# Performance work log

Hardware: AMD Instinct MI355X
Metric: run time of the kernel (lower is better)

The kernel has to match this reference:

```python
import jax, jax.numpy as jnp
import numpy as np

D = 1024      # atrybuty (d_model)
H = 16        # kanaly (heads)
DH = D // H   # head dim
B, T = 4, 2048
EPS = 1e-5


def setup_inputs() -> dict:
    key = jax.random.key(0)
    ks = jax.random.split(key, 16)
    s = 0.02
    return {
        "x":  jax.random.normal(ks[0], (B, T, D), jnp.float32),
        "wq": jax.random.normal(ks[1], (D, D), jnp.float32) * s,
        "wk": jax.random.normal(ks[2], (D, D), jnp.float32) * s,
        "wv": jax.random.normal(ks[3], (D, D), jnp.float32) * s,
        "wp": jax.random.normal(ks[4], (D, D), jnp.float32) * s,
        "bp": jnp.zeros((D,), jnp.float32),
        "w1": jax.random.normal(ks[5], (D, 4 * D), jnp.float32) * s,
        "b1": jnp.zeros((4 * D,), jnp.float32),
        "w2": jax.random.normal(ks[6], (4 * D, D), jnp.float32) * s,
        "b2": jnp.zeros((D,), jnp.float32),
        "g1": jnp.ones((D,), jnp.float32),
        "be1": jnp.zeros((D,), jnp.float32),
        "g2": jnp.ones((D,), jnp.float32),
        "be2": jnp.zeros((D,), jnp.float32),
    }


def _layernorm(x, g, b):
    mu = jnp.mean(x, axis=-1, keepdims=True)
    var = jnp.mean(jnp.square(x - mu), axis=-1, keepdims=True)
    return (x - mu) * jax.lax.rsqrt(var + EPS) * g + b


def reference(x, wq, wk, wv, wp, bp, w1, b1, w2, b2, g1, be1, g2, be2):
    b, t, d = x.shape
    # --- self-attention on ln1(x) ---
    h = _layernorm(x, g1, be1)
    # per-head Linears are equivalent to one [D,D] projection split into heads
    q = (h @ wq).reshape(b, t, H, DH).transpose(0, 2, 1, 3)  # [B,H,T,Dh]
    k = (h @ wk).reshape(b, t, H, DH).transpose(0, 2, 1, 3)
    v = (h @ wv).reshape(b, t, H, DH).transpose(0, 2, 1, 3)
    # NOTE: original scales by full embed dim C, not head_dim
    scale = jnp.asarray(d, x.dtype) ** -0.5
    wei = jnp.einsum("bhqd,bhkd->bhqk", q, k) * scale
    causal = jnp.tril(jnp.ones((t, t), bool))
    wei = jnp.where(causal, wei, -jnp.inf)
    wei = jax.nn.softmax(wei, axis=-1)
    att = jnp.einsum("bhqk,bhkd->bhqd", wei, v)
    att = att.transpose(0, 2, 1, 3).reshape(b, t, d)
    x = x + att @ wp + bp
    # --- feedforward on ln2(x) ---
    h2 = _layernorm(x, g2, be2)
    x = x + jax.nn.relu(h2 @ w1 + b1) @ w2 + b2
    return x
```

## Files before the change

kernel.cpp:

```cpp
#include <hip/hip_runtime.h>
#include <hip/hip_bf16.h>
#include <stdint.h>

#define DM   1024
#define NH   16
#define DH   64
#define BATCH 4
#define SEQ  2048
#define MROWS (BATCH*SEQ)

typedef float f32x4 __attribute__((ext_vector_type(4)));
typedef __bf16 bf16x8 __attribute__((ext_vector_type(8)));
typedef short s16x4 __attribute__((ext_vector_type(4)));
typedef int   i32x2 __attribute__((ext_vector_type(2)));

#define QSCALE 0.045084220f

#define VM(n) asm volatile("s_waitcnt vmcnt(" #n ")" ::: "memory")
#define LGKM0 do { asm volatile("s_waitcnt lgkmcnt(0)" ::: "memory"); \
                   __builtin_amdgcn_sched_barrier(0); } while (0)

__device__ __forceinline__ short f2bs(float f) {
    __bf16 h = (__bf16)f;
    return __builtin_bit_cast(short, h);
}

__device__ __forceinline__ void gload_lds16(const void* g, void* l) {
    __builtin_amdgcn_global_load_lds(
        (__attribute__((address_space(1))) void*)(g),
        (__attribute__((address_space(3))) void*)(l), 16, 0, 0);
}

__device__ __forceinline__ void swz_xy(int ny, int& x, int& y) {
    const int bid = blockIdx.x;
    const int cpx = gridDim.x >> 3;
    const int wg  = (bid & 7) * cpx + (bid >> 3);
    x = wg / ny;
    y = wg % ny;
}

__global__ __launch_bounds__(256) void transpose_cvt_kernel(
    const float* __restrict__ w, short* __restrict__ wt, int K, int N)
{
    __shared__ short tile[64 * 65];
    const int k0 = blockIdx.x * 64, n0 = blockIdx.y * 64;
    const int t = threadIdx.x;
#pragma unroll
    for (int i = 0; i < 16; ++i) {
        int idx = i * 256 + t;
        int r = idx >> 6, c = idx & 63;
        tile[r * 65 + c] = f2bs(w[(size_t)(k0 + r) * N + n0 + c]);
    }
    __syncthreads();
#pragma unroll
    for (int i = 0; i < 16; ++i) {
        int idx = i * 256 + t;
        int r = idx >> 6, c = idx & 63;
        wt[(size_t)(n0 + r) * K + k0 + c] = tile[c * 65 + r];
    }
}

__global__ __launch_bounds__(256) void ln_kernel(
    const float* __restrict__ x, const float* __restrict__ g,
    const float* __restrict__ be, short* __restrict__ out)
{
    const int row = blockIdx.x, t = threadIdx.x;
    const float4 v = ((const float4*)(x + (size_t)row * DM))[t];
    float s  = v.x + v.y + v.z + v.w;
    float ss = v.x * v.x + v.y * v.y + v.z * v.z + v.w * v.w;
#pragma unroll
    for (int d = 1; d < 64; d <<= 1) {
        s  += __shfl_xor(s, d, 64);
        ss += __shfl_xor(ss, d, 64);
    }
    __shared__ float red[8];
    const int wid = t >> 6;
    if ((t & 63) == 0) { red[wid] = s; red[wid + 4] = ss; }
    __syncthreads();
    s  = red[0] + red[1] + red[2] + red[3];
    ss = red[4] + red[5] + red[6] + red[7];
    const float mu = s * (1.0f / DM);
    const float rs = rsqrtf(ss * (1.0f / DM) - mu * mu + 1e-5f);
    const float4 gg = ((const float4*)g)[t];
    const float4 bb = ((const float4*)be)[t];
    short4 o;
    o.x = f2bs((v.x - mu) * rs * gg.x + bb.x);
    o.y = f2bs((v.y - mu) * rs * gg.y + bb.y);
    o.z = f2bs((v.z - mu) * rs * gg.z + bb.z);
    o.w = f2bs((v.w - mu) * rs * gg.w + bb.w);
    ((short4*)(out + (size_t)row * DM))[t] = o;
}

template<int NCHUNK>
__device__ __forceinline__ void stage32(
    const short* __restrict__ G, int ldk, int row0, int k0,
    short* __restrict__ lds, int t)
{
#pragma unroll
    for (int i = 0; i < NCHUNK / 512; ++i) {
        const int c  = i * 512 + t;
        const int r  = c >> 2;
        const int sl = (c & 3) ^ ((r >> 1) & 3);
        gload_lds16(&G[(size_t)(row0 + r) * ldk + k0 + sl * 8], &lds[c * 8]);
    }
}

template<int EPI>
__global__ __launch_bounds__(512) void gemm256(
    const short* __restrict__ A, const short* __restrict__ Bt,
    int N, int K, int nyT,
    const float* __restrict__ bias, short* __restrict__ outb,
    short* __restrict__ qo, short* __restrict__ ko, short* __restrict__ vo)
{
    __shared__ short As[4][8192];
    __shared__ short Bs[4][8192];
    const int t = threadIdx.x, lane = t & 63, w = t >> 6;
    const int l15 = lane & 15, hi = lane >> 4;
    const int wm = (w >> 2) * 128, wn = (w & 3) * 64;
    int bx, by; swz_xy(nyT, bx, by);
    const int m0 = bx * 256, n0 = by * 256;
    const int NT = K >> 5;

    f32x4 acc[8][4] = {};

    stage32<1024>(A, K, m0, 0,  As[0], t); stage32<1024>(Bt, K, n0, 0,  Bs[0], t);
    stage32<1024>(A, K, m0, 32, As[1], t); stage32<1024>(Bt, K, n0, 32, Bs[1], t);
    stage32<1024>(A, K, m0, 64, As[2], t); stage32<1024>(Bt, K, n0, 64, Bs[2], t);
    VM(8);
    __builtin_amdgcn_s_barrier();

    for (int kt = 0; kt < NT; ++kt) {
        const short* Ac = As[kt & 3];
        const short* Bc = Bs[kt & 3];
        const int k3 = (kt + 3) << 5;
        bf16x8 af[8], bfr[4];

#pragma unroll
        for (int fm = 0; fm < 4; ++fm) {
            const int r = wm + fm * 16 + l15;
            af[fm] = *(const bf16x8*)&Ac[r * 32 + ((hi ^ ((r >> 1) & 3)) << 3)];
        }
#pragma unroll
        for (int fn = 0; fn < 4; ++fn) {
            const int r = wn + fn * 16 + l15;
            bfr[fn] = *(const bf16x8*)&Bc[r * 32 + ((hi ^ ((r >> 1) & 3)) << 3)];
        }
        if (kt + 3 < NT) stage32<1024>(A, K, m0, k3, As[(kt + 3) & 3], t);
        __builtin_amdgcn_s_barrier();
        LGKM0;
        __builtin_amdgcn_s_setprio(1);
#pragma unroll
        for (int fm = 0; fm < 4; ++fm)
#pragma unroll
            for (int fn = 0; fn < 4; ++fn)
                acc[fm][fn] = __builtin_amdgcn_mfma_f32_16x16x32_bf16(
                    af[fm], bfr[fn], acc[fm][fn], 0, 0, 0);
        __builtin_amdgcn_s_setprio(0);
        __builtin_amdgcn_s_barrier();

#pragma unroll
        for (int fm = 4; fm < 8; ++fm) {
            const int r = wm + fm * 16 + l15;
            af[fm] = *(const bf16x8*)&Ac[r * 32 + ((hi ^ ((r >> 1) & 3)) << 3)];
        }
        if (kt + 3 < NT) {
            stage32<1024>(Bt, K, n0, k3, Bs[(kt + 3) & 3], t);
            VM(8);
        } else if (kt + 2 < NT) VM(4);
        else if (kt + 1 < NT) VM(0);
        __builtin_amdgcn_s_barrier();
        LGKM0;
        __builtin_amdgcn_s_setprio(1);
#pragma unroll
        for (int fm = 4; fm < 8; ++fm)
#pragma unroll
            for (int fn = 0; fn < 4; ++fn)
                acc[fm][fn] = __builtin_amdgcn_mfma_f32_16x16x32_bf16(
                    af[fm], bfr[fn], acc[fm][fn], 0, 0, 0);
        __builtin_amdgcn_s_setprio(0);
        __builtin_amdgcn_s_barrier();
    }

#pragma unroll
    for (int fm = 0; fm < 8; ++fm)
#pragma unroll
        for (int fn = 0; fn < 4; ++fn) {
            const int row0 = m0 + wm + fm * 16 + hi * 4;
            const int nn = n0 + wn + fn * 16 + l15;
            const f32x4 a = acc[fm][fn];
            if constexpr (EPI == 0) {
                const int mat = nn >> 10, n1 = nn & 1023;
                const int head = n1 >> 6, dh = n1 & 63;
                if (mat == 2) {
                    const int tok = row0 & 2047, b = row0 >> 11;
                    const int tokp = (tok & ~63) |
                        (((((tok >> 3) & 7) ^ (dh & 7)) << 3)) | (tok & 7);
                    short4 pk;
                    pk.x = f2bs(a[0]); pk.y = f2bs(a[1]);
                    pk.z = f2bs(a[2]); pk.w = f2bs(a[3]);
                    *(short4*)&vo[((size_t)(b * NH + head) * DH + dh) * SEQ + tokp] = pk;
                } else if (mat == 1) {
#pragma unroll
                    for (int rr = 0; rr < 4; ++rr) {
                        const int m = row0 + rr;
                        const int b = m >> 11, tok = m & 2047;
                        const int dhp = (((dh >> 3) ^ (tok & 7)) << 3) | (dh & 7);
                        ko[((size_t)(b * NH + head) * SEQ + tok) * DH + dhp] =
                            f2bs(a[rr]);
                    }
                } else {
#pragma unroll
                    for (int rr = 0; rr < 4; ++rr) {
                        const int m = row0 + rr;
                        const int b = m >> 11, tok = m & 2047;
                        qo[((size_t)(b * NH + head) * SEQ + tok) * DH + dh] =
                            f2bs(a[rr] * QSCALE);
                    }
                }
            } else {
                const float bb = bias[nn];
#pragma unroll
                for (int rr = 0; rr < 4; ++rr) {
                    const float z = a[rr] + bb;
                    outb[(size_t)(row0 + rr) * N + nn] = f2bs(z > 0.f ? z : 0.f);
                }
            }
        }
}

__global__ __launch_bounds__(256) void gemm_bt128(
    const short* __restrict__ A, const short* __restrict__ Bt,
    int N, int K, int nyT,
    const float* __restrict__ bias, const float* __restrict__ res,
    float* __restrict__ outf)
{
    __shared__ short As[4][4096];
    __shared__ short Bs[4][4096];
    const int t = threadIdx.x, lane = t & 63, w = t >> 6;
    const int l15 = lane & 15, hi = lane >> 4;
    const int wm = (w & 1) * 64, wn = (w >> 1) * 64;
    int bx, by; swz_xy(nyT, bx, by);
    const int m0 = bx * 128, n0 = by * 128;
    const int NT = K >> 5;

    f32x4 acc[4][4] = {};

#define STAGE128(G, row0, k0, lds)                                            \
    do {                                                                      \
        _Pragma("unroll")                                                     \
        for (int i2 = 0; i2 < 2; ++i2) {                                      \
            const int c  = i2 * 256 + t;                                      \
            const int r  = c >> 2;                                            \
            const int sl = (c & 3) ^ ((r >> 1) & 3);                          \
            gload_lds16(&(G)[(size_t)((row0) + r) * K + (k0) + sl * 8],       \
                        &(lds)[c * 8]);                                       \
        }                                                                     \
    } while (0)

    STAGE128(A, m0, 0,  As[0]); STAGE128(Bt, n0, 0,  Bs[0]);
    STAGE128(A, m0, 32, As[1]); STAGE128(Bt, n0, 32, Bs[1]);
    STAGE128(A, m0, 64, As[2]); STAGE128(Bt, n0, 64, Bs[2]);

    for (int kt = 0; kt < NT; ++kt) {
        if (kt + 3 < NT) {
            STAGE128(A,  m0, (kt + 3) << 5, As[(kt + 3) & 3]);
            STAGE128(Bt, n0, (kt + 3) << 5, Bs[(kt + 3) & 3]);
            VM(12);
        } else if (kt + 2 < NT) VM(8);
        else if (kt + 1 < NT) VM(4);
        else VM(0);
        __builtin_amdgcn_s_barrier();

        const short* Ac = As[kt & 3];
        const short* Bc = Bs[kt & 3];
        bf16x8 af[4], bfr[4];
#pragma unroll
        for (int fm = 0; fm < 4; ++fm) {
            const int r = wm + fm * 16 + l15;
            af[fm] = *(const bf16x8*)&Ac[r * 32 + ((hi ^ ((r >> 1) & 3)) << 3)];
        }
#pragma unroll
        for (int fn = 0; fn < 4; ++fn) {
            const int r = wn + fn * 16 + l15;
            bfr[fn] = *(const bf16x8*)&Bc[r * 32 + ((hi ^ ((r >> 1) & 3)) << 3)];
        }
        LGKM0;
        __builtin_amdgcn_s_barrier();

        __builtin_amdgcn_s_setprio(1);
#pragma unroll
        for (int fm = 0; fm < 4; ++fm)
#pragma unroll
            for (int fn = 0; fn < 4; ++fn)
                acc[fm][fn] = __builtin_amdgcn_mfma_f32_16x16x32_bf16(
                    af[fm], bfr[fn], acc[fm][fn], 0, 0, 0);
        __builtin_amdgcn_s_setprio(0);
    }
#undef STAGE128

#pragma unroll
    for (int fm = 0; fm < 4; ++fm)
#pragma unroll
        for (int fn = 0; fn < 4; ++fn) {
            const int row0 = m0 + wm + fm * 16 + hi * 4;
            const int nn = n0 + wn + fn * 16 + l15;
            const float bb = bias[nn];
            const f32x4 a = acc[fm][fn];
#pragma unroll
            for (int rr = 0; rr < 4; ++rr) {
                const int m = row0 + rr;
                outf[(size_t)m * N + nn] = a[rr] + bb + res[(size_t)m * N + nn];
            }
        }
}

__global__ __launch_bounds__(128) void attn_kernel(
    const short* __restrict__ Q, const short* __restrict__ Kx,
    const short* __restrict__ Vt, short* __restrict__ att)
{
    __shared__ short Ks[2][4096];
    __shared__ short Vs[2][4096];

    const int n  = blockIdx.x;
    const int bh = n & 63;
    const int qi = 31 - (n >> 6);
    const int tid = threadIdx.x;
    const int wv = tid >> 6;
    const int lane = tid & 63;
    const int l15 = lane & 15, hi = lane >> 4;
    const int q0 = qi * 64;
    const int qw = q0 + wv * 32;
    const size_t base  = (size_t)bh * (SEQ * DH);
    const size_t vbase = (size_t)bh * (DH * SEQ);
    const int b = bh >> 4, head = bh & 15;

    bf16x8 qf[2][2];
#pragma unroll
    for (int mf = 0; mf < 2; ++mf)
#pragma unroll
        for (int kf = 0; kf < 2; ++kf)
            qf[mf][kf] = *(const bf16x8*)
                &Q[base + (size_t)(qw + mf * 16 + l15) * DH + kf * 32 + hi * 8];

    f32x4 O[2][4] = {};
    float L[2] = {0.f, 0.f};

    const int nkv = qi + 1;

#define STAGE_KV(TT, BUF)                                                      \
    do {                                                                       \
        const int kvo = (TT) * 64;                                             \
        _Pragma("unroll")                                                      \
        for (int i2 = 0; i2 < 4; ++i2) {                                       \
            const int c = i2 * 128 + tid;                                      \
            const int rw = c >> 3, sl = c & 7;                                 \
            gload_lds16(&Kx[base + (size_t)(kvo + rw) * DH + sl * 8],          \
                        &Ks[BUF][c * 8]);                                      \
            gload_lds16(&Vt[vbase + (size_t)rw * SEQ + kvo + sl * 8],          \
                        &Vs[BUF][c * 8]);                                      \
        }                                                                      \
    } while (0)

    STAGE_KV(0, 0);

    for (int t2 = 0; t2 < nkv; ++t2) {
        if (t2 + 1 < nkv) { STAGE_KV(t2 + 1, (t2 + 1) & 1); VM(8); }
        else VM(0);
        __builtin_amdgcn_s_barrier();
        __builtin_amdgcn_sched_barrier(0);

        const short* Kc = Ks[t2 & 1];
        const short* Vc = Vs[t2 & 1];
        const int kv0 = t2 * 64;

        bf16x8 kfr[4][2];
#pragma unroll
        for (int nf = 0; nf < 4; ++nf)
#pragma unroll
            for (int kf = 0; kf < 2; ++kf)
                kfr[nf][kf] = *(const bf16x8*)
                    &Kc[(nf * 16 + l15) * 64 + (((kf * 4 + hi) ^ (l15 & 7)) << 3)];

        f32x4 St[4][2] = {};
#pragma unroll
        for (int kf = 0; kf < 2; ++kf)
#pragma unroll
            for (int nf = 0; nf < 4; ++nf)
#pragma unroll
                for (int mf = 0; mf < 2; ++mf)
                    St[nf][mf] = __builtin_amdgcn_mfma_f32_16x16x32_bf16(
                        kfr[nf][kf], qf[mf][kf], St[nf][mf], 0, 0, 0);

        if (kv0 + 63 > qw) {
#pragma unroll
            for (int mf = 0; mf < 2; ++mf) {
                const int q = qw + mf * 16 + l15;
#pragma unroll
                for (int nf = 0; nf < 4; ++nf)
#pragma unroll
                    for (int r = 0; r < 4; ++r) {
                        const int kv = kv0 + nf * 16 + hi * 4 + r;
                        if (kv > q) St[nf][mf][r] = -3.0e38f;
                    }
            }
        }

        s16x4 pa[4][2];
#pragma unroll
        for (int nf = 0; nf < 4; ++nf)
#pragma unroll
            for (int mf = 0; mf < 2; ++mf) {
                const float p0 = exp2f(St[nf][mf][0]);
                const float p1 = exp2f(St[nf][mf][1]);
                const float p2 = exp2f(St[nf][mf][2]);
                const float p3 = exp2f(St[nf][mf][3]);
                L[mf] += (p0 + p1) + (p2 + p3);
                unsigned dw0, dw1;
                asm("v_cvt_pk_bf16_f32 %0, %1, %2" : "=v"(dw0) : "v"(p0), "v"(p1));
                asm("v_cvt_pk_bf16_f32 %0, %1, %2" : "=v"(dw1) : "v"(p2), "v"(p3));
                i32x2 dd; dd[0] = (int)dw0; dd[1] = (int)dw1;
                pa[nf][mf] = __builtin_bit_cast(s16x4, dd);
            }

#pragma unroll
        for (int nf = 0; nf < 4; ++nf)
#pragma unroll
            for (int jf = 0; jf < 4; ++jf) {
                const s16x4 vfr = *(const s16x4*)
                    &Vc[(jf * 16 + l15) * 64 +
                        ((((nf * 2 + (hi >> 1)) ^ (l15 & 7)) << 3) + ((hi & 1) << 2))];
#pragma unroll
                for (int mf = 0; mf < 2; ++mf)
                    O[mf][jf] = __builtin_amdgcn_mfma_f32_16x16x16bf16_1k(
                        pa[nf][mf], vfr, O[mf][jf], 0, 0, 0);
            }

        __builtin_amdgcn_sched_barrier(0);
        __builtin_amdgcn_s_barrier();
    }
#undef STAGE_KV

#pragma unroll
    for (int mf = 0; mf < 2; ++mf) {
        L[mf] += __shfl_xor(L[mf], 16, 64);
        L[mf] += __shfl_xor(L[mf], 32, 64);
    }
    const float inv0 = 1.0f / L[0], inv1 = 1.0f / L[1];

#pragma unroll
    for (int mf = 0; mf < 2; ++mf) {
        const float invm = mf ? inv1 : inv0;
#pragma unroll
        for (int r = 0; r < 4; ++r) {
            const int addr = ((lane >> 4) << 4) + (r << 2);
            const float iv = __builtin_bit_cast(float,
                __builtin_amdgcn_ds_bpermute(addr, __builtin_bit_cast(int, invm)));
            const int q = qw + mf * 16 + hi * 4 + r;
#pragma unroll
            for (int jf = 0; jf < 4; ++jf)
                att[(size_t)(b * SEQ + q) * DM + head * DH + jf * 16 + l15] =
                    f2bs(O[mf][jf][r] * iv);
        }
    }
}

extern "C" void kernel_launch(void* const* d_in, const int* in_sizes, int n_in,
                              void* d_out, int out_size, void* d_ws, size_t ws_size,
                              hipStream_t stream) {
    const float* x   = (const float*)d_in[0];
    const float* wq  = (const float*)d_in[1];
    const float* wk  = (const float*)d_in[2];
    const float* wv  = (const float*)d_in[3];
    const float* wp  = (const float*)d_in[4];
    const float* bp  = (const float*)d_in[5];
    const float* w1  = (const float*)d_in[6];
    const float* b1  = (const float*)d_in[7];
    const float* w2  = (const float*)d_in[8];
    const float* b2  = (const float*)d_in[9];
    const float* g1  = (const float*)d_in[10];
    const float* be1 = (const float*)d_in[11];
    const float* g2  = (const float*)d_in[12];
    const float* be2 = (const float*)d_in[13];
    float* out = (float*)d_out;

    char* ws = (char*)d_ws;
    short* wqkv_t = (short*)(ws + 0);
    short* wp_t   = (short*)(ws + 6291456);
    short* w1_t   = (short*)(ws + 8388608);
    short* w2_t   = (short*)(ws + 16777216);
    short* h      = (short*)(ws + 25165824);
    short* qb     = (short*)(ws + 41943040);
    short* kb     = (short*)(ws + 58720256);
    short* vb     = (short*)(ws + 75497472);
    short* att    = (short*)(ws + 92274688);
    float* x1     = (float*)(ws + 109051904);
    short* h2     = (short*)(ws + 142606336);
    short* tbuf   = (short*)(ws + 25165824);

    dim3 blk(256);

    transpose_cvt_kernel<<<dim3(16, 16), blk, 0, stream>>>(wq, wqkv_t,                1024, 1024);
    transpose_cvt_kernel<<<dim3(16, 16), blk, 0, stream>>>(wk, wqkv_t + 1024 * 1024,  1024, 1024);
    transpose_cvt_kernel<<<dim3(16, 16), blk, 0, stream>>>(wv, wqkv_t + 2048 * 1024,  1024, 1024);
    transpose_cvt_kernel<<<dim3(16, 16), blk, 0, stream>>>(wp, wp_t,                  1024, 1024);
    transpose_cvt_kernel<<<dim3(16, 64), blk, 0, stream>>>(w1, w1_t,                  1024, 4096);
    transpose_cvt_kernel<<<dim3(64, 16), blk, 0, stream>>>(w2, w2_t,                  4096, 1024);

    ln_kernel<<<MROWS, blk, 0, stream>>>(x, g1, be1, h);

    gemm256<0><<<dim3(384), dim3(512), 0, stream>>>(h, wqkv_t, 3072, 1024, 12,
        nullptr, nullptr, qb, kb, vb);

    attn_kernel<<<dim3(2048), dim3(128), 0, stream>>>(qb, kb, vb, att);

    gemm_bt128<<<dim3(512), blk, 0, stream>>>(att, wp_t, 1024, 1024, 8,
        bp, x, x1);

    ln_kernel<<<MROWS, blk, 0, stream>>>(x1, g2, be2, h2);

    gemm256<2><<<dim3(512), dim3(512), 0, stream>>>(h2, w1_t, 4096, 1024, 16,
        b1, tbuf, nullptr, nullptr, nullptr);

    gemm_bt128<<<dim3(512), blk, 0, stream>>>(tbuf, w2_t, 1024, 4096, 8,
        b2, x1, out);
}
```

Before: 394.8 us.

## Simplify GEMM main loops to a single wait-barrier-compute-stage schedule

Both bf16 GEMM kernels drop the hand-interleaved schedule, which split the MFMA work into two halves, issued global-to-LDS loads mid-iteration, used explicit lgkmcnt waits with sched barriers and raised wave priority around the MFMAs. Each iteration now waits on vmcnt, runs one barrier, reads all fragments, does all MFMAs, then uses a second barrier before staging tile kt+3. This lets the compiler schedule LDS reads and MFMAs freely and cuts barriers per iteration. It may lose overlap between global loads and compute, and it holds more fragment registers live at once.

```diff
diff --git a/kernel.cpp b/kernel.cpp
--- a/kernel.cpp
+++ b/kernel.cpp
@@ -17,8 +17,6 @@
 #define QSCALE 0.045084220f
 
 #define VM(n) asm volatile("s_waitcnt vmcnt(" #n ")" ::: "memory")
-#define LGKM0 do { asm volatile("s_waitcnt lgkmcnt(0)" ::: "memory"); \
-                   __builtin_amdgcn_sched_barrier(0); } while (0)
 
 __device__ __forceinline__ short f2bs(float f) {
     __bf16 h = (__bf16)f;
@@ -126,17 +124,18 @@
     stage32<1024>(A, K, m0, 0,  As[0], t); stage32<1024>(Bt, K, n0, 0,  Bs[0], t);
     stage32<1024>(A, K, m0, 32, As[1], t); stage32<1024>(Bt, K, n0, 32, Bs[1], t);
     stage32<1024>(A, K, m0, 64, As[2], t); stage32<1024>(Bt, K, n0, 64, Bs[2], t);
-    VM(8);
-    __builtin_amdgcn_s_barrier();
 
     for (int kt = 0; kt < NT; ++kt) {
+        if (kt + 2 < NT) VM(8);
+        else if (kt + 1 < NT) VM(4);
+        else VM(0);
+        __builtin_amdgcn_s_barrier();
+
         const short* Ac = As[kt & 3];
         const short* Bc = Bs[kt & 3];
-        const int k3 = (kt + 3) << 5;
         bf16x8 af[8], bfr[4];
-
-#pragma unroll
-        for (int fm = 0; fm < 4; ++fm) {
+#pragma unroll
+        for (int fm = 0; fm < 8; ++fm) {
             const int r = wm + fm * 16 + l15;
             af[fm] = *(const bf16x8*)&Ac[r * 32 + ((hi ^ ((r >> 1) & 3)) << 3)];
         }
@@ -145,40 +144,19 @@
             const int r = wn + fn * 16 + l15;
             bfr[fn] = *(const bf16x8*)&Bc[r * 32 + ((hi ^ ((r >> 1) & 3)) << 3)];
         }
-        if (kt + 3 < NT) stage32<1024>(A, K, m0, k3, As[(kt + 3) & 3], t);
-        __builtin_amdgcn_s_barrier();
-        LGKM0;
-        __builtin_amdgcn_s_setprio(1);
-#pragma unroll
-        for (int fm = 0; fm < 4; ++fm)
+#pragma unroll
+        for (int fm = 0; fm < 8; ++fm)
 #pragma unroll
             for (int fn = 0; fn < 4; ++fn)
                 acc[fm][fn] = __builtin_amdgcn_mfma_f32_16x16x32_bf16(
                     af[fm], bfr[fn], acc[fm][fn], 0, 0, 0);
-        __builtin_amdgcn_s_setprio(0);
+
         __builtin_amdgcn_s_barrier();
-
-#pragma unroll
-        for (int fm = 4; fm < 8; ++fm) {
-            const int r = wm + fm * 16 + l15;
-            af[fm] = *(const bf16x8*)&Ac[r * 32 + ((hi ^ ((r >> 1) & 3)) << 3)];
-        }
         if (kt + 3 < NT) {
+            const int k3 = (kt + 3) << 5;
+            stage32<1024>(A,  K, m0, k3, As[(kt + 3) & 3], t);
             stage32<1024>(Bt, K, n0, k3, Bs[(kt + 3) & 3], t);
-            VM(8);
-        } else if (kt + 2 < NT) VM(4);
-        else if (kt + 1 < NT) VM(0);
-        __builtin_amdgcn_s_barrier();
-        LGKM0;
-        __builtin_amdgcn_s_setprio(1);
-#pragma unroll
-        for (int fm = 4; fm < 8; ++fm)
-#pragma unroll
-            for (int fn = 0; fn < 4; ++fn)
-                acc[fm][fn] = __builtin_amdgcn_mfma_f32_16x16x32_bf16(
-                    af[fm], bfr[fn], acc[fm][fn], 0, 0, 0);
-        __builtin_amdgcn_s_setprio(0);
-        __builtin_amdgcn_s_barrier();
+        }
     }
 
 #pragma unroll
@@ -262,39 +240,36 @@
     STAGE128(A, m0, 64, As[2]); STAGE128(Bt, n0, 64, Bs[2]);
 
     for (int kt = 0; kt < NT; ++kt) {
+        if (kt + 2 < NT) VM(8);
+        else if (kt + 1 < NT) VM(4);
+        else VM(0);
+        __builtin_amdgcn_s_barrier();
+
+        const short* Ac = As[kt & 3];
+        const short* Bc = Bs[kt & 3];
+        bf16x8 af[4], bfr[4];
+#pragma unroll
+        for (int fm = 0; fm < 4; ++fm) {
+            const int r = wm + fm * 16 + l15;
+            af[fm] = *(const bf16x8*)&Ac[r * 32 + ((hi ^ ((r >> 1) & 3)) << 3)];
+        }
+#pragma unroll
+        for (int fn = 0; fn < 4; ++fn) {
+            const int r = wn + fn * 16 + l15;
+            bfr[fn] = *(const bf16x8*)&Bc[r * 32 + ((hi ^ ((r >> 1) & 3)) << 3)];
+        }
+#pragma unroll
+        for (int fm = 0; fm < 4; ++fm)
+#pragma unroll
+            for (int fn = 0; fn < 4; ++fn)
+                acc[fm][fn] = __builtin_amdgcn_mfma_f32_16x16x32_bf16(
+                    af[fm], bfr[fn], acc[fm][fn], 0, 0, 0);
+
+        __builtin_amdgcn_s_barrier();
         if (kt + 3 < NT) {
             STAGE128(A,  m0, (kt + 3) << 5, As[(kt + 3) & 3]);
             STAGE128(Bt, n0, (kt + 3) << 5, Bs[(kt + 3) & 3]);
-            VM(12);
-        } else if (kt + 2 < NT) VM(8);
-        else if (kt + 1 < NT) VM(4);
-        else VM(0);
-        __builtin_amdgcn_s_barrier();
-
-        const short* Ac = As[kt & 3];
-        const short* Bc = Bs[kt & 3];
-        bf16x8 af[4], bfr[4];
-#pragma unroll
-        for (int fm = 0; fm < 4; ++fm) {
-            const int r = wm + fm * 16 + l15;
-            af[fm] = *(const bf16x8*)&Ac[r * 32 + ((hi ^ ((r >> 1) & 3)) << 3)];
-        }
-#pragma unroll
-        for (int fn = 0; fn < 4; ++fn) {
-            const int r = wn + fn * 16 + l15;
-            bfr[fn] = *(const bf16x8*)&Bc[r * 32 + ((hi ^ ((r >> 1) & 3)) << 3)];
-        }
-        LGKM0;
-        __builtin_amdgcn_s_barrier();
-
-        __builtin_amdgcn_s_setprio(1);
-#pragma unroll
-        for (int fm = 0; fm < 4; ++fm)
-#pragma unroll
-            for (int fn = 0; fn < 4; ++fn)
-                acc[fm][fn] = __builtin_amdgcn_mfma_f32_16x16x32_bf16(
-                    af[fm], bfr[fn], acc[fm][fn], 0, 0, 0);
-        __builtin_amdgcn_s_setprio(0);
+        }
     }
 #undef STAGE128
 
```

After: 406.1 us. 1.03x slower.
